# Kernel tuning notes

Hardware: AMD Instinct MI355X
Metric: run time of the kernel (lower is better)

The kernel has to match this reference:

```python
import jax, jax.numpy as jnp
import numpy as np

NUM_HEADS = 16
WINDOW = 256
DIM = 1024


def setup_inputs() -> dict:
    key = jax.random.key(0)
    k1, k2, k3, k4, k5 = jax.random.split(key, 5)
    B, L, D = 2, 2048, DIM
    s = 1.0 / np.sqrt(D)
    return {
        "x": jax.random.normal(k1, (B, L, D), dtype=jnp.float32),
        "in_proj_w": jax.random.uniform(k2, (3 * D, D), dtype=jnp.float32, minval=-s, maxval=s),
        "in_proj_b": jax.random.uniform(k3, (3 * D,), dtype=jnp.float32, minval=-s, maxval=s),
        "out_w": jax.random.uniform(k4, (D, D), dtype=jnp.float32, minval=-s, maxval=s),
        "out_b": jax.random.uniform(k5, (D,), dtype=jnp.float32, minval=-s, maxval=s),
    }


def reference(x, in_proj_w, in_proj_b, out_w, out_b):
    B, L, D = x.shape
    H = NUM_HEADS
    hd = D // H

    # combined qkv projection, as in nn.MultiheadAttention
    qkv = x @ in_proj_w.T + in_proj_b          # [B, L, 3D]
    q, k, v = jnp.split(qkv, 3, axis=-1)
    q = q.reshape(B, L, H, hd).transpose(0, 2, 1, 3)  # [B, H, L, hd]
    k = k.reshape(B, L, H, hd).transpose(0, 2, 1, 3)
    v = v.reshape(B, L, H, hd).transpose(0, 2, 1, 3)

    scale = 1.0 / jnp.sqrt(jnp.asarray(hd, dtype=x.dtype))
    scores = jnp.einsum("bhqd,bhkd->bhqk", q * scale, k)  # [B, H, L, L]

    # sliding-window causal mask: allowed iff i-window < j <= i
    i = jnp.arange(L)[:, None]
    j = jnp.arange(L)[None, :]
    allowed = (j <= i) & (j > i - WINDOW)                  # [L, L]
    scores = jnp.where(allowed[None, None], scores, -jnp.inf)

    attn = jax.nn.softmax(scores, axis=-1)
    out = jnp.einsum("bhqk,bhkd->bhqd", attn, v)           # [B, H, L, hd]
    out = out.transpose(0, 2, 1, 3).reshape(B, L, D)
    return out @ out_w.T + out_b
```

## Files before the change

kernel.cpp:

```cpp
#include <hip/hip_runtime.h>


#define SEQ_L 2048
#define WIN   256

typedef __bf16 bf16x8 __attribute__((ext_vector_type(8)));
typedef float  f32x4  __attribute__((ext_vector_type(4)));

__device__ __forceinline__ unsigned short f32_to_bf16(float f) {
  return (unsigned short)((__float_as_uint(f) + 0x8000u) >> 16);
}

__device__ __forceinline__ void async16(const unsigned short* g, unsigned short* l) {
  __builtin_amdgcn_global_load_lds(
      (const __attribute__((address_space(1))) unsigned int*)g,
      (__attribute__((address_space(3))) unsigned int*)l, 16, 0, 0);
}

__global__ void cast_all(const float* __restrict__ x,  unsigned short* __restrict__ xo,
                         const float* __restrict__ w1, unsigned short* __restrict__ w1o,
                         const float* __restrict__ w2, unsigned short* __restrict__ w2o) {
  int i = blockIdx.x * 256 + threadIdx.x;
  const float* in; unsigned short* out; int k;
  if (i < 1048576)       { in = x;  out = xo;  k = i; }
  else if (i < 1835008)  { in = w1; out = w1o; k = i - 1048576; }
  else                   { in = w2; out = w2o; k = i - 1835008; }
  float4 v = ((const float4*)in)[k];
  ushort4 o;
  o.x = f32_to_bf16(v.x); o.y = f32_to_bf16(v.y);
  o.z = f32_to_bf16(v.z); o.w = f32_to_bf16(v.w);
  ((ushort4*)out)[k] = o;
}

template<int TBM, int TBN, int MI, int NI, int OUTBF>
__global__ __launch_bounds__(256) void gemm_nt(
    const unsigned short* __restrict__ A,
    const unsigned short* __restrict__ Bt,
    const float* __restrict__ bias,
    void* __restrict__ Cout, int M, int N, int K)
{
  __shared__ unsigned short As[TBM * 64];
  __shared__ unsigned short Bs[TBN * 64];

  const int tid  = threadIdx.x;
  const int lane = tid & 63;
  const int wave = tid >> 6;
  const int wr   = (wave >> 1) * (MI * 16);
  const int wc   = (wave & 1) * (NI * 16);
  const int quad = lane >> 4;
  const int l16  = lane & 15;
  const int lrow = lane >> 3;
  const int scol = (lane & 7) ^ lrow;

  const long m0 = (long)blockIdx.y * TBM;
  const long n0 = (long)blockIdx.x * TBN;

  f32x4 acc[MI][NI];
#pragma unroll
  for (int i = 0; i < MI; ++i)
#pragma unroll
    for (int j = 0; j < NI; ++j)
#pragma unroll
      for (int r = 0; r < 4; ++r) acc[i][j][r] = 0.0f;

  for (int k0 = 0; k0 < K; k0 += 64) {
#pragma unroll
    for (int p = 0; p < TBM / 32; ++p) {
      int rb = wave * (TBM / 4) + p * 8;
      async16(A + (m0 + rb + lrow) * (long)K + k0 + scol * 8, &As[rb * 64]);
    }
#pragma unroll
    for (int p = 0; p < TBN / 32; ++p) {
      int rb = wave * (TBN / 4) + p * 8;
      async16(Bt + (n0 + rb + lrow) * (long)K + k0 + scol * 8, &Bs[rb * 64]);
    }
    __syncthreads();
#pragma unroll
    for (int ks = 0; ks < 2; ++ks) {
      bf16x8 af[MI], bfv[NI];
#pragma unroll
      for (int mi = 0; mi < MI; ++mi) {
        int r = wr + mi * 16 + l16;
        af[mi] = *(const bf16x8*)(&As[r * 64 + ((ks * 4 + quad) ^ (r & 7)) * 8]);
      }
#pragma unroll
      for (int ni = 0; ni < NI; ++ni) {
        int r = wc + ni * 16 + l16;
        bfv[ni] = *(const bf16x8*)(&Bs[r * 64 + ((ks * 4 + quad) ^ (r & 7)) * 8]);
      }
#pragma unroll
      for (int mi = 0; mi < MI; ++mi)
#pragma unroll
        for (int ni = 0; ni < NI; ++ni)
          acc[mi][ni] = __builtin_amdgcn_mfma_f32_16x16x32_bf16(af[mi], bfv[ni], acc[mi][ni], 0, 0, 0);
    }
    __syncthreads();
  }

#pragma unroll
  for (int ni = 0; ni < NI; ++ni) {
    long col = n0 + wc + ni * 16 + l16;
    float bv = bias[col];
#pragma unroll
    for (int mi = 0; mi < MI; ++mi) {
      long rowb = m0 + wr + mi * 16 + quad * 4;
#pragma unroll
      for (int r = 0; r < 4; ++r) {
        float v = acc[mi][ni][r] + bv;
        if (OUTBF) ((unsigned short*)Cout)[(rowb + r) * N + col] = f32_to_bf16(v);
        else       ((float*)Cout)[(rowb + r) * N + col] = v;
      }
    }
  }
}

__global__ __launch_bounds__(256) void attn_kernel(
    const unsigned short* __restrict__ qkv,
    unsigned short* __restrict__ aout)
{
  __shared__ unsigned short Ks[64 * 72];
  __shared__ unsigned short Vt[64 * 72];
  __shared__ unsigned short Ps[4 * 16 * 72];

  const int tid  = threadIdx.x;
  const int w    = tid >> 6;
  const int lane = tid & 63;
  const int quad = lane >> 4;
  const int l16  = lane & 15;

  const int blk = blockIdx.x;
  const int qb  = blk & 15;
  const int h   = (blk >> 4) & 15;
  const int b   = blk >> 8;

  const int  i0 = qb * 128;
  const long rowbase = (long)b * SEQ_L;
  const float C_EXP = 0.18033688f;

  bf16x8 ones;
#pragma unroll
  for (int e = 0; e < 8; ++e) ones[e] = (__bf16)1.0f;

  bf16x8 aq[2][2];
#pragma unroll
  for (int sub = 0; sub < 2; ++sub) {
    const unsigned short* qp =
        qkv + (rowbase + i0 + sub * 64 + w * 16 + l16) * 3072 + h * 64 + quad * 8;
    aq[sub][0] = *(const bf16x8*)(qp);
    aq[sub][1] = *(const bf16x8*)(qp + 32);
  }

  f32x4 o[2][4], ol[2];
#pragma unroll
  for (int sub = 0; sub < 2; ++sub) {
#pragma unroll
    for (int r = 0; r < 4; ++r) ol[sub][r] = 0.0f;
#pragma unroll
    for (int ni = 0; ni < 4; ++ni)
#pragma unroll
      for (int r = 0; r < 4; ++r) o[sub][ni][r] = 0.0f;
  }

  unsigned short* psw = &Ps[w * 16 * 72];
  const int j_begin = (i0 >= WIN) ? i0 - WIN : 0;

  for (int j0 = j_begin; j0 < i0 + 128; j0 += 64) {
    __syncthreads();
#pragma unroll
    for (int p = 0; p < 2; ++p) {
      int c = p * 256 + tid, row = c >> 3, col8 = c & 7;
      const unsigned short* base = qkv + (rowbase + j0 + row) * 3072 + h * 64 + col8 * 8;
      *(uint4*)(&Ks[row * 72 + col8 * 8]) = *(const uint4*)(base + 1024);
      unsigned short tmp[8];
      *(uint4*)tmp = *(const uint4*)(base + 2048);
      int rsw = row ^ (col8 << 3);
#pragma unroll
      for (int e = 0; e < 8; ++e)
        Vt[(col8 * 8 + e) * 72 + rsw] = tmp[e];
    }
    __syncthreads();

    bf16x8 kf[4][2];
#pragma unroll
    for (int g = 0; g < 4; ++g) {
      kf[g][0] = *(const bf16x8*)(&Ks[(g * 16 + l16) * 72 + quad * 8]);
      kf[g][1] = *(const bf16x8*)(&Ks[(g * 16 + l16) * 72 + 32 + quad * 8]);
    }
    bf16x8 vf[2][4];
#pragma unroll
    for (int kk = 0; kk < 2; ++kk)
#pragma unroll
      for (int ni = 0; ni < 4; ++ni) {
        int d  = ni * 16 + l16;
        int rb = (kk * 32 + quad * 8) ^ (((d >> 3) & 7) << 3);
        vf[kk][ni] = *(const bf16x8*)(&Vt[d * 72 + rb]);
      }

#pragma unroll
    for (int sub = 0; sub < 2; ++sub) {
      const int i0s = i0 + sub * 64 + w * 16;
      if (j0 > i0s + 15) continue;
      if (j0 + 63 + WIN <= i0s) continue;

#pragma unroll
      for (int g = 0; g < 4; ++g) {
        const int jmin = j0 + g * 16, jmax = jmin + 15;
        if (jmin > i0s + 15 || jmax + WIN <= i0s) {
#pragma unroll
          for (int r = 0; r < 4; ++r)
            psw[(quad * 4 + r) * 72 + g * 16 + l16] = 0;
          continue;
        }
        f32x4 z;
#pragma unroll
        for (int r = 0; r < 4; ++r) z[r] = 0.0f;
        z = __builtin_amdgcn_mfma_f32_16x16x32_bf16(aq[sub][0], kf[g][0], z, 0, 0, 0);
        z = __builtin_amdgcn_mfma_f32_16x16x32_bf16(aq[sub][1], kf[g][1], z, 0, 0, 0);
        const bool full = (jmax <= i0s) && (jmin + WIN > i0s + 15);
        if (full) {
#pragma unroll
          for (int r = 0; r < 4; ++r)
            psw[(quad * 4 + r) * 72 + g * 16 + l16] =
                f32_to_bf16(__builtin_exp2f(z[r] * C_EXP));
        } else {
          const int j = jmin + l16;
#pragma unroll
          for (int r = 0; r < 4; ++r) {
            int i = i0s + quad * 4 + r;
            bool ok = (j <= i) && (j > i - WIN);
            float e = ok ? __builtin_exp2f(z[r] * C_EXP) : 0.0f;
            psw[(quad * 4 + r) * 72 + g * 16 + l16] = f32_to_bf16(e);
          }
        }
      }
      asm volatile("s_waitcnt lgkmcnt(0)" ::: "memory");
#pragma unroll
      for (int kk = 0; kk < 2; ++kk) {
        bf16x8 ap = *(const bf16x8*)(&psw[l16 * 72 + kk * 32 + quad * 8]);
        ol[sub] = __builtin_amdgcn_mfma_f32_16x16x32_bf16(ap, ones, ol[sub], 0, 0, 0);
#pragma unroll
        for (int ni = 0; ni < 4; ++ni)
          o[sub][ni] = __builtin_amdgcn_mfma_f32_16x16x32_bf16(ap, vf[kk][ni], o[sub][ni], 0, 0, 0);
      }
    }
  }

#pragma unroll
  for (int sub = 0; sub < 2; ++sub)
#pragma unroll
    for (int r = 0; r < 4; ++r) {
      float inv_l = 1.0f / ol[sub][r];
      long row = rowbase + i0 + sub * 64 + w * 16 + quad * 4 + r;
#pragma unroll
      for (int ni = 0; ni < 4; ++ni)
        aout[row * 1024 + h * 64 + ni * 16 + l16] = f32_to_bf16(o[sub][ni][r] * inv_l);
    }
}

extern "C" void kernel_launch(void* const* d_in, const int* in_sizes, int n_in,
                              void* d_out, int out_size, void* d_ws, size_t ws_size,
                              hipStream_t stream)
{
  const float* x  = (const float*)d_in[0];
  const float* w1 = (const float*)d_in[1];
  const float* b1 = (const float*)d_in[2];
  const float* w2 = (const float*)d_in[3];
  const float* b2 = (const float*)d_in[4];
  float* out = (float*)d_out;

  char* ws = (char*)d_ws;
  unsigned short* x_bf   = (unsigned short*)(ws);
  unsigned short* w1_bf  = (unsigned short*)(ws + 8388608);
  unsigned short* w2_bf  = (unsigned short*)(ws + 14680064);
  unsigned short* qkv_bf = (unsigned short*)(ws + 16777216);
  unsigned short* at_bf  = (unsigned short*)(ws + 41943040);

  cast_all<<<8192, 256, 0, stream>>>(x, x_bf, w1, w1_bf, w2, w2_bf);

  dim3 g1(1536 / 128, 4096 / 128);
  gemm_nt<128, 128, 4, 4, 1><<<g1, 256, 0, stream>>>(
      x_bf, w1_bf, b1, qkv_bf, 4096, 3072, 1024);
  gemm_nt<128, 128, 4, 4, 1><<<g1, 256, 0, stream>>>(
      x_bf, w1_bf + 1536 * 1024, b1 + 1536, qkv_bf + 1536, 4096, 3072, 1024);

  attn_kernel<<<512, 256, 0, stream>>>(qkv_bf, at_bf);

  dim3 g2(1024 / 64, 4096 / 64);
  gemm_nt<64, 64, 2, 2, 0><<<g2, 256, 0, stream>>>(at_bf, w2_bf, b2, out, 4096, 1024, 1024);
}
```

Baseline: 172.8 us.

## Fuse all stages into one persistent cooperative kernel with grid barriers

Replaces the five separate launches (cast, two QKV GEMMs, attention, output GEMM) with a single persistent cooperative kernel. Blocks loop over work tiles and synchronise between stages with an atomic grid barrier, so per-launch overhead and inter-kernel gaps go away. The output projection tile changes from 64x64 to 128x64. In exchange the grid is capped at 3 blocks per CU, which can reduce occupancy for the attention and GEMM phases. The design also relies on cooperative launch, and a multi-kernel fallback runs if that launch fails.

```diff
diff --git a/kernel.cpp b/kernel.cpp
--- a/kernel.cpp
+++ b/kernel.cpp
@@ -15,6 +15,284 @@
   __builtin_amdgcn_global_load_lds(
       (const __attribute__((address_space(1))) unsigned int*)g,
       (__attribute__((address_space(3))) unsigned int*)l, 16, 0, 0);
+}
+
+__device__ __forceinline__ void gridbar(unsigned* cnt, unsigned* gen) {
+  __syncthreads();
+  __threadfence();
+  if (threadIdx.x == 0) {
+    unsigned g = __hip_atomic_load(gen, __ATOMIC_RELAXED, __HIP_MEMORY_SCOPE_AGENT);
+    unsigned a = __hip_atomic_fetch_add(cnt, 1u, __ATOMIC_ACQ_REL, __HIP_MEMORY_SCOPE_AGENT);
+    if (a + 1 == gridDim.x) {
+      __hip_atomic_store(cnt, 0u, __ATOMIC_RELAXED, __HIP_MEMORY_SCOPE_AGENT);
+      __hip_atomic_fetch_add(gen, 1u, __ATOMIC_ACQ_REL, __HIP_MEMORY_SCOPE_AGENT);
+    } else {
+      while (__hip_atomic_load(gen, __ATOMIC_ACQUIRE, __HIP_MEMORY_SCOPE_AGENT) == g)
+        __builtin_amdgcn_s_sleep(8);
+    }
+  }
+  __syncthreads();
+  __threadfence();
+}
+
+template<int TBM, int TBN, int MI, int NI, int OUTBF>
+__device__ __forceinline__ void gemm_tile(
+    const unsigned short* __restrict__ A,
+    const unsigned short* __restrict__ Bt,
+    const float* __restrict__ bias,
+    void* __restrict__ Cout, int N, int K, int bx, int by,
+    unsigned short* As, unsigned short* Bs)
+{
+  const int tid  = threadIdx.x;
+  const int lane = tid & 63;
+  const int wave = tid >> 6;
+  const int wr   = (wave >> 1) * (MI * 16);
+  const int wc   = (wave & 1) * (NI * 16);
+  const int quad = lane >> 4;
+  const int l16  = lane & 15;
+  const int lrow = lane >> 3;
+  const int scol = (lane & 7) ^ lrow;
+
+  const long m0 = (long)by * TBM;
+  const long n0 = (long)bx * TBN;
+
+  f32x4 acc[MI][NI];
+#pragma unroll
+  for (int i = 0; i < MI; ++i)
+#pragma unroll
+    for (int j = 0; j < NI; ++j)
+#pragma unroll
+      for (int r = 0; r < 4; ++r) acc[i][j][r] = 0.0f;
+
+  for (int k0 = 0; k0 < K; k0 += 64) {
+#pragma unroll
+    for (int p = 0; p < TBM / 32; ++p) {
+      int rb = wave * (TBM / 4) + p * 8;
+      async16(A + (m0 + rb + lrow) * (long)K + k0 + scol * 8, &As[rb * 64]);
+    }
+#pragma unroll
+    for (int p = 0; p < TBN / 32; ++p) {
+      int rb = wave * (TBN / 4) + p * 8;
+      async16(Bt + (n0 + rb + lrow) * (long)K + k0 + scol * 8, &Bs[rb * 64]);
+    }
+    __syncthreads();
+#pragma unroll
+    for (int ks = 0; ks < 2; ++ks) {
+      bf16x8 af[MI], bfv[NI];
+#pragma unroll
+      for (int mi = 0; mi < MI; ++mi) {
+        int r = wr + mi * 16 + l16;
+        af[mi] = *(const bf16x8*)(&As[r * 64 + ((ks * 4 + quad) ^ (r & 7)) * 8]);
+      }
+#pragma unroll
+      for (int ni = 0; ni < NI; ++ni) {
+        int r = wc + ni * 16 + l16;
+        bfv[ni] = *(const bf16x8*)(&Bs[r * 64 + ((ks * 4 + quad) ^ (r & 7)) * 8]);
+      }
+#pragma unroll
+      for (int mi = 0; mi < MI; ++mi)
+#pragma unroll
+        for (int ni = 0; ni < NI; ++ni)
+          acc[mi][ni] = __builtin_amdgcn_mfma_f32_16x16x32_bf16(af[mi], bfv[ni], acc[mi][ni], 0, 0, 0);
+    }
+    __syncthreads();
+  }
+
+#pragma unroll
+  for (int ni = 0; ni < NI; ++ni) {
+    long col = n0 + wc + ni * 16 + l16;
+    float bv = bias[col];
+#pragma unroll
+    for (int mi = 0; mi < MI; ++mi) {
+      long rowb = m0 + wr + mi * 16 + quad * 4;
+#pragma unroll
+      for (int r = 0; r < 4; ++r) {
+        float v = acc[mi][ni][r] + bv;
+        if (OUTBF) ((unsigned short*)Cout)[(rowb + r) * N + col] = f32_to_bf16(v);
+        else       ((float*)Cout)[(rowb + r) * N + col] = v;
+      }
+    }
+  }
+}
+
+__device__ __forceinline__ void attn_unit(
+    const unsigned short* __restrict__ qkv,
+    unsigned short* __restrict__ aout, int unit, char* smem)
+{
+  unsigned short* Ks = (unsigned short*)smem;
+  unsigned short* Vt = (unsigned short*)(smem + 9216);
+  unsigned short* Ps = (unsigned short*)(smem + 18432);
+
+  const int tid  = threadIdx.x;
+  const int w    = tid >> 6;
+  const int lane = tid & 63;
+  const int quad = lane >> 4;
+  const int l16  = lane & 15;
+
+  const int qb = unit & 15;
+  const int h  = (unit >> 4) & 15;
+  const int b  = unit >> 8;
+
+  const int  i0 = qb * 128;
+  const long rowbase = (long)b * SEQ_L;
+  const float C_EXP = 0.18033688f;
+
+  bf16x8 ones;
+#pragma unroll
+  for (int e = 0; e < 8; ++e) ones[e] = (__bf16)1.0f;
+
+  bf16x8 aq[2][2];
+#pragma unroll
+  for (int sub = 0; sub < 2; ++sub) {
+    const unsigned short* qp =
+        qkv + (rowbase + i0 + sub * 64 + w * 16 + l16) * 3072 + h * 64 + quad * 8;
+    aq[sub][0] = *(const bf16x8*)(qp);
+    aq[sub][1] = *(const bf16x8*)(qp + 32);
+  }
+
+  f32x4 o[2][4], ol[2];
+#pragma unroll
+  for (int sub = 0; sub < 2; ++sub) {
+#pragma unroll
+    for (int r = 0; r < 4; ++r) ol[sub][r] = 0.0f;
+#pragma unroll
+    for (int ni = 0; ni < 4; ++ni)
+#pragma unroll
+      for (int r = 0; r < 4; ++r) o[sub][ni][r] = 0.0f;
+  }
+
+  unsigned short* psw = &Ps[w * 16 * 72];
+  const int j_begin = (i0 >= WIN) ? i0 - WIN : 0;
+
+  for (int j0 = j_begin; j0 < i0 + 128; j0 += 64) {
+    __syncthreads();
+#pragma unroll
+    for (int p = 0; p < 2; ++p) {
+      int c = p * 256 + tid, row = c >> 3, col8 = c & 7;
+      const unsigned short* base = qkv + (rowbase + j0 + row) * 3072 + h * 64 + col8 * 8;
+      *(uint4*)(&Ks[row * 72 + col8 * 8]) = *(const uint4*)(base + 1024);
+      unsigned short tmp[8];
+      *(uint4*)tmp = *(const uint4*)(base + 2048);
+      int rsw = row ^ (col8 << 3);
+#pragma unroll
+      for (int e = 0; e < 8; ++e)
+        Vt[(col8 * 8 + e) * 72 + rsw] = tmp[e];
+    }
+    __syncthreads();
+
+    bf16x8 kf[4][2];
+#pragma unroll
+    for (int g = 0; g < 4; ++g) {
+      kf[g][0] = *(const bf16x8*)(&Ks[(g * 16 + l16) * 72 + quad * 8]);
+      kf[g][1] = *(const bf16x8*)(&Ks[(g * 16 + l16) * 72 + 32 + quad * 8]);
+    }
+    bf16x8 vf[2][4];
+#pragma unroll
+    for (int kk = 0; kk < 2; ++kk)
+#pragma unroll
+      for (int ni = 0; ni < 4; ++ni) {
+        int d  = ni * 16 + l16;
+        int rb = (kk * 32 + quad * 8) ^ (((d >> 3) & 7) << 3);
+        vf[kk][ni] = *(const bf16x8*)(&Vt[d * 72 + rb]);
+      }
+
+#pragma unroll
+    for (int sub = 0; sub < 2; ++sub) {
+      const int i0s = i0 + sub * 64 + w * 16;
+      if (j0 > i0s + 15) continue;
+      if (j0 + 63 + WIN <= i0s) continue;
+
+#pragma unroll
+      for (int g = 0; g < 4; ++g) {
+        const int jmin = j0 + g * 16, jmax = jmin + 15;
+        if (jmin > i0s + 15 || jmax + WIN <= i0s) {
+#pragma unroll
+          for (int r = 0; r < 4; ++r)
+            psw[(quad * 4 + r) * 72 + g * 16 + l16] = 0;
+          continue;
+        }
+        f32x4 z;
+#pragma unroll
+        for (int r = 0; r < 4; ++r) z[r] = 0.0f;
+        z = __builtin_amdgcn_mfma_f32_16x16x32_bf16(aq[sub][0], kf[g][0], z, 0, 0, 0);
+        z = __builtin_amdgcn_mfma_f32_16x16x32_bf16(aq[sub][1], kf[g][1], z, 0, 0, 0);
+        const bool full = (jmax <= i0s) && (jmin + WIN > i0s + 15);
+        if (full) {
+#pragma unroll
+          for (int r = 0; r < 4; ++r)
+            psw[(quad * 4 + r) * 72 + g * 16 + l16] =
+                f32_to_bf16(__builtin_exp2f(z[r] * C_EXP));
+        } else {
+          const int j = jmin + l16;
+#pragma unroll
+          for (int r = 0; r < 4; ++r) {
+            int i = i0s + quad * 4 + r;
+            bool ok = (j <= i) && (j > i - WIN);
+            float e = ok ? __builtin_exp2f(z[r] * C_EXP) : 0.0f;
+            psw[(quad * 4 + r) * 72 + g * 16 + l16] = f32_to_bf16(e);
+          }
+        }
+      }
+      asm volatile("s_waitcnt lgkmcnt(0)" ::: "memory");
+#pragma unroll
+      for (int kk = 0; kk < 2; ++kk) {
+        bf16x8 ap = *(const bf16x8*)(&psw[l16 * 72 + kk * 32 + quad * 8]);
+        ol[sub] = __builtin_amdgcn_mfma_f32_16x16x32_bf16(ap, ones, ol[sub], 0, 0, 0);
+#pragma unroll
+        for (int ni = 0; ni < 4; ++ni)
+          o[sub][ni] = __builtin_amdgcn_mfma_f32_16x16x32_bf16(ap, vf[kk][ni], o[sub][ni], 0, 0, 0);
+      }
+    }
+  }
+
+#pragma unroll
+  for (int sub = 0; sub < 2; ++sub)
+#pragma unroll
+    for (int r = 0; r < 4; ++r) {
+      float inv_l = 1.0f / ol[sub][r];
+      long row = rowbase + i0 + sub * 64 + w * 16 + quad * 4 + r;
+#pragma unroll
+      for (int ni = 0; ni < 4; ++ni)
+        aout[row * 1024 + h * 64 + ni * 16 + l16] = f32_to_bf16(o[sub][ni][r] * inv_l);
+    }
+}
+
+__global__ __launch_bounds__(256, 3) void fused_all(
+    const float* __restrict__ x,  const float* __restrict__ w1,
+    const float* __restrict__ b1, const float* __restrict__ w2,
+    const float* __restrict__ b2,
+    unsigned short* xbf, unsigned short* w1bf, unsigned short* w2bf,
+    unsigned short* qkv, unsigned short* at, float* out, unsigned* bar)
+{
+  __shared__ __align__(16) char smem[32768];
+  const int blk = blockIdx.x, tid = threadIdx.x;
+  const int G = gridDim.x;
+
+  for (int i = blk * 256 + tid; i < 2097152; i += G * 256) {
+    const float* in; unsigned short* o; int k;
+    if (i < 1048576)      { in = x;  o = xbf;  k = i; }
+    else if (i < 1835008) { in = w1; o = w1bf; k = i - 1048576; }
+    else                  { in = w2; o = w2bf; k = i - 1835008; }
+    float4 v = ((const float4*)in)[k];
+    ushort4 u;
+    u.x = f32_to_bf16(v.x); u.y = f32_to_bf16(v.y);
+    u.z = f32_to_bf16(v.z); u.w = f32_to_bf16(v.w);
+    ((ushort4*)o)[k] = u;
+  }
+  gridbar(bar, bar + 1);
+
+  for (int t = blk; t < 768; t += G)
+    gemm_tile<128, 128, 4, 4, 1>(xbf, w1bf, b1, qkv, 3072, 1024, t % 24, t / 24,
+                                 (unsigned short*)smem, (unsigned short*)(smem + 16384));
+  gridbar(bar, bar + 1);
+
+  for (int t = blk; t < 512; t += G)
+    attn_unit(qkv, at, t, smem);
+  gridbar(bar, bar + 1);
+
+  for (int t = blk; t < 512; t += G)
+    gemm_tile<128, 64, 4, 2, 0>(at, w2bf, b2, out, 1024, 1024, t % 16, t / 16,
+                                (unsigned short*)smem, (unsigned short*)(smem + 16384));
 }
 
 __global__ void cast_all(const float* __restrict__ x,  unsigned short* __restrict__ xo,
@@ -34,227 +312,20 @@
 
 template<int TBM, int TBN, int MI, int NI, int OUTBF>
 __global__ __launch_bounds__(256) void gemm_nt(
-    const unsigned short* __restrict__ A,
-    const unsigned short* __restrict__ Bt,
-    const float* __restrict__ bias,
-    void* __restrict__ Cout, int M, int N, int K)
+    const unsigned short* __restrict__ A, const unsigned short* __restrict__ Bt,
+    const float* __restrict__ bias, void* __restrict__ Cout, int N, int K)
 {
   __shared__ unsigned short As[TBM * 64];
   __shared__ unsigned short Bs[TBN * 64];
-
-  const int tid  = threadIdx.x;
-  const int lane = tid & 63;
-  const int wave = tid >> 6;
-  const int wr   = (wave >> 1) * (MI * 16);
-  const int wc   = (wave & 1) * (NI * 16);
-  const int quad = lane >> 4;
-  const int l16  = lane & 15;
-  const int lrow = lane >> 3;
-  const int scol = (lane & 7) ^ lrow;
-
-  const long m0 = (long)blockIdx.y * TBM;
-  const long n0 = (long)blockIdx.x * TBN;
-
-  f32x4 acc[MI][NI];
-#pragma unroll
-  for (int i = 0; i < MI; ++i)
-#pragma unroll
-    for (int j = 0; j < NI; ++j)
-#pragma unroll
-      for (int r = 0; r < 4; ++r) acc[i][j][r] = 0.0f;
-
-  for (int k0 = 0; k0 < K; k0 += 64) {
-#pragma unroll
-    for (int p = 0; p < TBM / 32; ++p) {
-      int rb = wave * (TBM / 4) + p * 8;
-      async16(A + (m0 + rb + lrow) * (long)K + k0 + scol * 8, &As[rb * 64]);
-    }
-#pragma unroll
-    for (int p = 0; p < TBN / 32; ++p) {
-      int rb = wave * (TBN / 4) + p * 8;
-      async16(Bt + (n0 + rb + lrow) * (long)K + k0 + scol * 8, &Bs[rb * 64]);
-    }
-    __syncthreads();
-#pragma unroll
-    for (int ks = 0; ks < 2; ++ks) {
-      bf16x8 af[MI], bfv[NI];
-#pragma unroll
-      for (int mi = 0; mi < MI; ++mi) {
-        int r = wr + mi * 16 + l16;
-        af[mi] = *(const bf16x8*)(&As[r * 64 + ((ks * 4 + quad) ^ (r & 7)) * 8]);
-      }
-#pragma unroll
-      for (int ni = 0; ni < NI; ++ni) {
-        int r = wc + ni * 16 + l16;
-        bfv[ni] = *(const bf16x8*)(&Bs[r * 64 + ((ks * 4 + quad) ^ (r & 7)) * 8]);
-      }
-#pragma unroll
-      for (int mi = 0; mi < MI; ++mi)
-#pragma unroll
-        for (int ni = 0; ni < NI; ++ni)
-          acc[mi][ni] = __builtin_amdgcn_mfma_f32_16x16x32_bf16(af[mi], bfv[ni], acc[mi][ni], 0, 0, 0);
-    }
-    __syncthreads();
-  }
-
-#pragma unroll
-  for (int ni = 0; ni < NI; ++ni) {
-    long col = n0 + wc + ni * 16 + l16;
-    float bv = bias[col];
-#pragma unroll
-    for (int mi = 0; mi < MI; ++mi) {
-      long rowb = m0 + wr + mi * 16 + quad * 4;
-#pragma unroll
-      for (int r = 0; r < 4; ++r) {
-        float v = acc[mi][ni][r] + bv;
-        if (OUTBF) ((unsigned short*)Cout)[(rowb + r) * N + col] = f32_to_bf16(v);
-        else       ((float*)Cout)[(rowb + r) * N + col] = v;
-      }
-    }
-  }
+  gemm_tile<TBM, TBN, MI, NI, OUTBF>(A, Bt, bias, Cout, N, K,
+                                     blockIdx.x, blockIdx.y, As, Bs);
 }
 
 __global__ __launch_bounds__(256) void attn_kernel(
-    const unsigned short* __restrict__ qkv,
-    unsigned short* __restrict__ aout)
-{
-  __shared__ unsigned short Ks[64 * 72];
-  __shared__ unsigned short Vt[64 * 72];
-  __shared__ unsigned short Ps[4 * 16 * 72];
-
-  const int tid  = threadIdx.x;
-  const int w    = tid >> 6;
-  const int lane = tid & 63;
-  const int quad = lane >> 4;
-  const int l16  = lane & 15;
-
-  const int blk = blockIdx.x;
-  const int qb  = blk & 15;
-  const int h   = (blk >> 4) & 15;
-  const int b   = blk >> 8;
-
-  const int  i0 = qb * 128;
-  const long rowbase = (long)b * SEQ_L;
-  const float C_EXP = 0.18033688f;
-
-  bf16x8 ones;
-#pragma unroll
-  for (int e = 0; e < 8; ++e) ones[e] = (__bf16)1.0f;
-
-  bf16x8 aq[2][2];
-#pragma unroll
-  for (int sub = 0; sub < 2; ++sub) {
-    const unsigned short* qp =
-        qkv + (rowbase + i0 + sub * 64 + w * 16 + l16) * 3072 + h * 64 + quad * 8;
-    aq[sub][0] = *(const bf16x8*)(qp);
-    aq[sub][1] = *(const bf16x8*)(qp + 32);
-  }
-
-  f32x4 o[2][4], ol[2];
-#pragma unroll
-  for (int sub = 0; sub < 2; ++sub) {
-#pragma unroll
-    for (int r = 0; r < 4; ++r) ol[sub][r] = 0.0f;
-#pragma unroll
-    for (int ni = 0; ni < 4; ++ni)
-#pragma unroll
-      for (int r = 0; r < 4; ++r) o[sub][ni][r] = 0.0f;
-  }
-
-  unsigned short* psw = &Ps[w * 16 * 72];
-  const int j_begin = (i0 >= WIN) ? i0 - WIN : 0;
-
-  for (int j0 = j_begin; j0 < i0 + 128; j0 += 64) {
-    __syncthreads();
-#pragma unroll
-    for (int p = 0; p < 2; ++p) {
-      int c = p * 256 + tid, row = c >> 3, col8 = c & 7;
-      const unsigned short* base = qkv + (rowbase + j0 + row) * 3072 + h * 64 + col8 * 8;
-      *(uint4*)(&Ks[row * 72 + col8 * 8]) = *(const uint4*)(base + 1024);
-      unsigned short tmp[8];
-      *(uint4*)tmp = *(const uint4*)(base + 2048);
-      int rsw = row ^ (col8 << 3);
-#pragma unroll
-      for (int e = 0; e < 8; ++e)
-        Vt[(col8 * 8 + e) * 72 + rsw] = tmp[e];
-    }
-    __syncthreads();
-
-    bf16x8 kf[4][2];
-#pragma unroll
-    for (int g = 0; g < 4; ++g) {
-      kf[g][0] = *(const bf16x8*)(&Ks[(g * 16 + l16) * 72 + quad * 8]);
-      kf[g][1] = *(const bf16x8*)(&Ks[(g * 16 + l16) * 72 + 32 + quad * 8]);
-    }
-    bf16x8 vf[2][4];
-#pragma unroll
-    for (int kk = 0; kk < 2; ++kk)
-#pragma unroll
-      for (int ni = 0; ni < 4; ++ni) {
-        int d  = ni * 16 + l16;
-        int rb = (kk * 32 + quad * 8) ^ (((d >> 3) & 7) << 3);
-        vf[kk][ni] = *(const bf16x8*)(&Vt[d * 72 + rb]);
-      }
-
-#pragma unroll
-    for (int sub = 0; sub < 2; ++sub) {
-      const int i0s = i0 + sub * 64 + w * 16;
-      if (j0 > i0s + 15) continue;
-      if (j0 + 63 + WIN <= i0s) continue;
-
-#pragma unroll
-      for (int g = 0; g < 4; ++g) {
-        const int jmin = j0 + g * 16, jmax = jmin + 15;
-        if (jmin > i0s + 15 || jmax + WIN <= i0s) {
-#pragma unroll
-          for (int r = 0; r < 4; ++r)
-            psw[(quad * 4 + r) * 72 + g * 16 + l16] = 0;
-          continue;
-        }
-        f32x4 z;
-#pragma unroll
-        for (int r = 0; r < 4; ++r) z[r] = 0.0f;
-        z = __builtin_amdgcn_mfma_f32_16x16x32_bf16(aq[sub][0], kf[g][0], z, 0, 0, 0);
-        z = __builtin_amdgcn_mfma_f32_16x16x32_bf16(aq[sub][1], kf[g][1], z, 0, 0, 0);
-        const bool full = (jmax <= i0s) && (jmin + WIN > i0s + 15);
-        if (full) {
-#pragma unroll
-          for (int r = 0; r < 4; ++r)
-            psw[(quad * 4 + r) * 72 + g * 16 + l16] =
-                f32_to_bf16(__builtin_exp2f(z[r] * C_EXP));
-        } else {
-          const int j = jmin + l16;
-#pragma unroll
-          for (int r = 0; r < 4; ++r) {
-            int i = i0s + quad * 4 + r;
-            bool ok = (j <= i) && (j > i - WIN);
-            float e = ok ? __builtin_exp2f(z[r] * C_EXP) : 0.0f;
-            psw[(quad * 4 + r) * 72 + g * 16 + l16] = f32_to_bf16(e);
-          }
-        }
-      }
-      asm volatile("s_waitcnt lgkmcnt(0)" ::: "memory");
-#pragma unroll
-      for (int kk = 0; kk < 2; ++kk) {
-        bf16x8 ap = *(const bf16x8*)(&psw[l16 * 72 + kk * 32 + quad * 8]);
-        ol[sub] = __builtin_amdgcn_mfma_f32_16x16x32_bf16(ap, ones, ol[sub], 0, 0, 0);
-#pragma unroll
-        for (int ni = 0; ni < 4; ++ni)
-          o[sub][ni] = __builtin_amdgcn_mfma_f32_16x16x32_bf16(ap, vf[kk][ni], o[sub][ni], 0, 0, 0);
-      }
-    }
-  }
-
-#pragma unroll
-  for (int sub = 0; sub < 2; ++sub)
-#pragma unroll
-    for (int r = 0; r < 4; ++r) {
-      float inv_l = 1.0f / ol[sub][r];
-      long row = rowbase + i0 + sub * 64 + w * 16 + quad * 4 + r;
-#pragma unroll
-      for (int ni = 0; ni < 4; ++ni)
-        aout[row * 1024 + h * 64 + ni * 16 + l16] = f32_to_bf16(o[sub][ni][r] * inv_l);
-    }
+    const unsigned short* __restrict__ qkv, unsigned short* __restrict__ aout)
+{
+  __shared__ __align__(16) char smem[27648];
+  attn_unit(qkv, aout, blockIdx.x, smem);
 }
 
 extern "C" void kernel_launch(void* const* d_in, const int* in_sizes, int n_in,
@@ -274,17 +345,28 @@
   unsigned short* w2_bf  = (unsigned short*)(ws + 14680064);
   unsigned short* qkv_bf = (unsigned short*)(ws + 16777216);
   unsigned short* at_bf  = (unsigned short*)(ws + 41943040);
-
-  cast_all<<<8192, 256, 0, stream>>>(x, x_bf, w1, w1_bf, w2, w2_bf);
-
-  dim3 g1(1536 / 128, 4096 / 128);
-  gemm_nt<128, 128, 4, 4, 1><<<g1, 256, 0, stream>>>(
-      x_bf, w1_bf, b1, qkv_bf, 4096, 3072, 1024);
-  gemm_nt<128, 128, 4, 4, 1><<<g1, 256, 0, stream>>>(
-      x_bf, w1_bf + 1536 * 1024, b1 + 1536, qkv_bf + 1536, 4096, 3072, 1024);
-
-  attn_kernel<<<512, 256, 0, stream>>>(qkv_bf, at_bf);
-
-  dim3 g2(1024 / 64, 4096 / 64);
-  gemm_nt<64, 64, 2, 2, 0><<<g2, 256, 0, stream>>>(at_bf, w2_bf, b2, out, 4096, 1024, 1024);
-}
+  unsigned*       bar    = (unsigned*)(ws + 50331648);
+
+  hipMemsetAsync(bar, 0, 256, stream);
+
+  int maxb = 0;
+  hipError_t qerr = hipOccupancyMaxActiveBlocksPerMultiprocessor(
+      &maxb, (const void*)fused_all, 256, 0);
+  int blkpc = (qerr == hipSuccess && maxb > 0) ? (maxb < 3 ? maxb : 3) : 3;
+  dim3 grid(blkpc * 256);
+
+  void* args[] = { (void*)&x, (void*)&w1, (void*)&b1, (void*)&w2, (void*)&b2,
+                   (void*)&x_bf, (void*)&w1_bf, (void*)&w2_bf,
+                   (void*)&qkv_bf, (void*)&at_bf, (void*)&out, (void*)&bar };
+  hipError_t err = hipLaunchCooperativeKernel(
+      (const void*)fused_all, grid, dim3(256), args, 0, stream);
+
+  if (err != hipSuccess) {
+    cast_all<<<8192, 256, 0, stream>>>(x, x_bf, w1, w1_bf, w2, w2_bf);
+    dim3 g1(24, 32);
+    gemm_nt<128, 128, 4, 4, 1><<<g1, 256, 0, stream>>>(x_bf, w1_bf, b1, qkv_bf, 3072, 1024);
+    attn_kernel<<<512, 256, 0, stream>>>(qkv_bf, at_bf);
+    dim3 g2(16, 32);
+    gemm_nt<128, 64, 4, 2, 0><<<g2, 256, 0, stream>>>(at_bf, w2_bf, b2, out, 1024, 1024);
+  }
+}
```

After: 471.3 us. 2.73x slower.

## Fuse fp32-to-bf16 conversion into GEMM tile loads, drop separate cast kernel

Applied to the files above, without the earlier changes.

Removes the standalone cast kernel. The GEMMs now load fp32 x and weights directly, convert them to bf16 in registers and store them into LDS, instead of going through a bf16 staging buffer. The QKV projection becomes one launch over all 3072 columns instead of two. This saves a kernel launch and a full write-and-reread of the bf16 copies. In exchange, the GEMM reads twice the global bytes per tile and loses the async global-to-LDS load path, and each weight element is converted once per M-tile rather than once overall.

```diff
diff --git a/kernel.cpp b/kernel.cpp
--- a/kernel.cpp
+++ b/kernel.cpp
@@ -17,27 +17,24 @@
       (__attribute__((address_space(3))) unsigned int*)l, 16, 0, 0);
 }
 
-__global__ void cast_all(const float* __restrict__ x,  unsigned short* __restrict__ xo,
-                         const float* __restrict__ w1, unsigned short* __restrict__ w1o,
-                         const float* __restrict__ w2, unsigned short* __restrict__ w2o) {
-  int i = blockIdx.x * 256 + threadIdx.x;
-  const float* in; unsigned short* out; int k;
-  if (i < 1048576)       { in = x;  out = xo;  k = i; }
-  else if (i < 1835008)  { in = w1; out = w1o; k = i - 1048576; }
-  else                   { in = w2; out = w2o; k = i - 1835008; }
-  float4 v = ((const float4*)in)[k];
-  ushort4 o;
-  o.x = f32_to_bf16(v.x); o.y = f32_to_bf16(v.y);
-  o.z = f32_to_bf16(v.z); o.w = f32_to_bf16(v.w);
-  ((ushort4*)out)[k] = o;
-}
-
-template<int TBM, int TBN, int MI, int NI, int OUTBF>
+__device__ __forceinline__ void stage8_cvt(const float* __restrict__ g,
+                                           unsigned short* l) {
+  float4 f0 = ((const float4*)g)[0];
+  float4 f1 = ((const float4*)g)[1];
+  ushort4 u0, u1;
+  u0.x = f32_to_bf16(f0.x); u0.y = f32_to_bf16(f0.y);
+  u0.z = f32_to_bf16(f0.z); u0.w = f32_to_bf16(f0.w);
+  u1.x = f32_to_bf16(f1.x); u1.y = f32_to_bf16(f1.y);
+  u1.z = f32_to_bf16(f1.z); u1.w = f32_to_bf16(f1.w);
+  ((ushort4*)l)[0] = u0;
+  ((ushort4*)l)[1] = u1;
+}
+
+template<int TBM, int TBN, int MI, int NI, int OUTBF, int ACVT, int BCVT>
 __global__ __launch_bounds__(256) void gemm_nt(
-    const unsigned short* __restrict__ A,
-    const unsigned short* __restrict__ Bt,
+    const void* __restrict__ Ain, const void* __restrict__ Btin,
     const float* __restrict__ bias,
-    void* __restrict__ Cout, int M, int N, int K)
+    void* __restrict__ Cout, int N, int K)
 {
   __shared__ unsigned short As[TBM * 64];
   __shared__ unsigned short Bs[TBN * 64];
@@ -67,12 +64,22 @@
 #pragma unroll
     for (int p = 0; p < TBM / 32; ++p) {
       int rb = wave * (TBM / 4) + p * 8;
-      async16(A + (m0 + rb + lrow) * (long)K + k0 + scol * 8, &As[rb * 64]);
+      if (ACVT)
+        stage8_cvt((const float*)Ain + (m0 + rb + lrow) * (long)K + k0 + scol * 8,
+                   &As[(rb + lrow) * 64 + (lane & 7) * 8]);
+      else
+        async16((const unsigned short*)Ain + (m0 + rb + lrow) * (long)K + k0 + scol * 8,
+                &As[rb * 64]);
     }
 #pragma unroll
     for (int p = 0; p < TBN / 32; ++p) {
       int rb = wave * (TBN / 4) + p * 8;
-      async16(Bt + (n0 + rb + lrow) * (long)K + k0 + scol * 8, &Bs[rb * 64]);
+      if (BCVT)
+        stage8_cvt((const float*)Btin + (n0 + rb + lrow) * (long)K + k0 + scol * 8,
+                   &Bs[(rb + lrow) * 64 + (lane & 7) * 8]);
+      else
+        async16((const unsigned short*)Btin + (n0 + rb + lrow) * (long)K + k0 + scol * 8,
+                &Bs[rb * 64]);
     }
     __syncthreads();
 #pragma unroll
@@ -269,22 +276,16 @@
   float* out = (float*)d_out;
 
   char* ws = (char*)d_ws;
-  unsigned short* x_bf   = (unsigned short*)(ws);
-  unsigned short* w1_bf  = (unsigned short*)(ws + 8388608);
-  unsigned short* w2_bf  = (unsigned short*)(ws + 14680064);
-  unsigned short* qkv_bf = (unsigned short*)(ws + 16777216);
-  unsigned short* at_bf  = (unsigned short*)(ws + 41943040);
-
-  cast_all<<<8192, 256, 0, stream>>>(x, x_bf, w1, w1_bf, w2, w2_bf);
-
-  dim3 g1(1536 / 128, 4096 / 128);
-  gemm_nt<128, 128, 4, 4, 1><<<g1, 256, 0, stream>>>(
-      x_bf, w1_bf, b1, qkv_bf, 4096, 3072, 1024);
-  gemm_nt<128, 128, 4, 4, 1><<<g1, 256, 0, stream>>>(
-      x_bf, w1_bf + 1536 * 1024, b1 + 1536, qkv_bf + 1536, 4096, 3072, 1024);
+  unsigned short* qkv_bf = (unsigned short*)(ws);
+  unsigned short* at_bf  = (unsigned short*)(ws + 25165824);
+
+  dim3 g1(3072 / 128, 4096 / 128);
+  gemm_nt<128, 128, 4, 4, 1, 1, 1><<<g1, 256, 0, stream>>>(
+      x, w1, b1, qkv_bf, 3072, 1024);
 
   attn_kernel<<<512, 256, 0, stream>>>(qkv_bf, at_bf);
 
   dim3 g2(1024 / 64, 4096 / 64);
-  gemm_nt<64, 64, 2, 2, 0><<<g2, 256, 0, stream>>>(at_bf, w2_bf, b2, out, 4096, 1024, 1024);
-}
+  gemm_nt<64, 64, 2, 2, 0, 0, 1><<<g2, 256, 0, stream>>>(
+      at_bf, w2, b2, out, 1024, 1024);
+}
```

After: 174.9 us. No clear change (+1.2%).
